# Kernel tuning notes

Hardware: AMD Instinct MI355X
Metric: run time of the kernel (lower is better)

The kernel has to match this reference:

```python
import jax, jax.numpy as jnp
import numpy as np

EPS = 1e-12  # F.normalize eps


def setup_inputs() -> dict:
    key = jax.random.key(0)
    k1, k2 = jax.random.split(key)
    bs, d = 8192, 128
    data = jax.random.normal(k1, (bs, d), dtype=jnp.float32)
    label = jax.random.randint(k2, (bs, 1), 0, 2, dtype=jnp.int64)
    scale = jnp.asarray(np.log(1.0 / 0.07), dtype=jnp.float32)  # learned temperature param
    return {"data": data, "scale": scale, "label": label}


def reference(data, scale, label):
    bs = data.shape[0]
    # L2-normalize rows (F.normalize semantics with eps clamp)
    norm = jnp.maximum(jnp.linalg.norm(data, axis=-1, keepdims=True), EPS)
    x = data / norm
    logits = (x @ x.T) * jnp.exp(scale)  # [bs, bs]
    # Vectorized equivalent of the python double loop: binary same-class matrix
    sim = (label == label.T).astype(logits.dtype)  # [bs, bs]
    q = jax.nn.softmax(sim / jnp.sum(sim, axis=-1, keepdims=True), axis=-1)
    p = jax.nn.log_softmax(logits, axis=-1)
    log_q = jnp.log(q)  # q > 0 always (softmax output)
    # F.kl_div(p, q, 'batchmean') = sum(q * (log q - p)) / bs
    loss1 = jnp.sum(q * (log_q - p)) / bs
    # F.kl_div(q.log(), p.exp(), 'batchmean') = sum(exp(p) * (p - log q)) / bs
    loss2 = jnp.sum(jnp.exp(p) * (p - log_q)) / bs
    return (loss1 + loss2) * 0.5
```

## Files before the change

kernel.cpp:

```cpp
#include <hip/hip_runtime.h>
#include <stdint.h>

#define BS 8192
#define DD 128
#define L2E 1.4426950408889634f
#define LN2 0.6931471805599453f

typedef __attribute__((ext_vector_type(8))) short short8;
typedef __attribute__((ext_vector_type(4))) float float4v;

#if __has_builtin(__builtin_amdgcn_exp2f)
#define EXP2(x) __builtin_amdgcn_exp2f(x)
#else
#define EXP2(x) exp2f(x)
#endif

__device__ __forceinline__ float bf2f(short s) {
  union { unsigned u; float f; } c;
  c.u = ((unsigned)(unsigned short)s) << 16;
  return c.f;
}
__device__ __forceinline__ short f2bf(float f) {
  union { float f; unsigned u; } c; c.f = f;
  unsigned u = c.u + 0x7FFFu + ((c.u >> 16) & 1u);
  return (short)(u >> 16);
}


__global__ __launch_bounds__(256) void k_norm(const float* __restrict__ data,
                                              const int* __restrict__ label,
                                              char* __restrict__ xnbF,
                                              float* __restrict__ Zr,
                                              float* __restrict__ Ur,
                                              float* __restrict__ Vr,
                                              float* __restrict__ Wr,
                                              float* __restrict__ Xr,
                                              float* __restrict__ mf) {
  int tid = threadIdx.x, wave = tid >> 6, lane = tid & 63;
  int lh = lane & 31, rsel = lane >> 5;
  int rowbase = blockIdx.x * 16;
  if (tid < 16) {
    int row = rowbase + tid;
    Zr[row] = 0.f; Ur[row] = 0.f; Vr[row] = 0.f; Wr[row] = 0.f; Xr[row] = 0.f;
    mf[row] = (label[row] == 0) ? 1.f : 0.f;
  }
#pragma unroll
  for (int it = 0; it < 2; ++it) {
    int row = rowbase + it * 8 + wave * 2 + rsel;
    float4 v = *(const float4*)&data[row * DD + lh * 4];
    float ss = v.x * v.x + v.y * v.y + v.z * v.z + v.w * v.w;
#pragma unroll
    for (int off = 16; off; off >>= 1) ss += __shfl_xor(ss, off);
    float rn = 1.f / fmaxf(sqrtf(ss), 1e-12f);
    float x0 = v.x * rn, x1 = v.y * rn, x2 = v.z * rn, x3 = v.w * rn;

    unsigned pk0 = (unsigned)(unsigned short)f2bf(x0) |
                   ((unsigned)(unsigned short)f2bf(x1) << 16);
    unsigned pk1 = (unsigned)(unsigned short)f2bf(x2) |
                   ((unsigned)(unsigned short)f2bf(x3) << 16);
    int kc = lh >> 1;
    size_t chunk = (size_t)(row >> 4) * 256 + (size_t)(kc >> 2) * 64 +
                   (size_t)(kc & 3) * 16 + (row & 15);
    *(uint2*)(xnbF + chunk * 16 + (lh & 1) * 8) = make_uint2(pk0, pk1);
  }
}

__global__ __launch_bounds__(512, 4) void k_main(const short* __restrict__ xnbF,
                                                 const int* __restrict__ label,
                                                 const float* __restrict__ mf,
                                                 const float* __restrict__ scale,
                                                 float* __restrict__ Zr,
                                                 float* __restrict__ Ur,
                                                 float* __restrict__ Vr,
                                                 float* __restrict__ Wr,
                                                 float* __restrict__ Xr,
                                                 int* __restrict__ ticket,
                                                 float* __restrict__ out) {
  __shared__ short tile[2][64 * DD];
  __shared__ int credu[8];
  __shared__ float fredu[8];
  __shared__ int lastf;
  int tid = threadIdx.x, wave = tid >> 6, lane = tid & 63;
  int quad = lane >> 4, col = lane & 15;
  int rbI = blockIdx.x >> 4;
  int sl = blockIdx.x & 15;
  float se2 = __expf(scale[0]) * L2E;

  const short8* F = (const short8*)xnbF;
  int gA = rbI * 16 + wave * 2;
  short8 af[2][4];
#pragma unroll
  for (int s = 0; s < 2; ++s)
#pragma unroll
    for (int t = 0; t < 4; ++t) {
      short8 a = F[(size_t)(gA + s) * 256 + t * 64 + lane];
#pragma unroll
      for (int i = 0; i < 8; ++i) a[i] = f2bf(bf2f(a[i]) * se2);
      af[s][t] = a;
    }

  float4v Z0 = {0.f,0.f,0.f,0.f}, Z1 = Z0, U0 = Z0, U1 = Z0, V0 = Z0, V1 = Z0;
  float4v W0 = Z0, W1 = Z0, X0 = Z0, X1 = Z0;
  int cb4 = sl * 32;

#define STAGE(buf, jt)                                                         \
  {                                                                            \
    const char* s_ = (const char*)xnbF +                                       \
                     ((size_t)(cb4 + (jt) * 4) * 256 + tid) * 16;              \
    char* d_ = (char*)tile[buf] + tid * 16;                                    \
    __builtin_amdgcn_global_load_lds(                                          \
        (const __attribute__((address_space(1))) void*)(uintptr_t)s_,          \
        (__attribute__((address_space(3))) void*)(uintptr_t)d_, 16, 0, 0);     \
    __builtin_amdgcn_global_load_lds(                                          \
        (const __attribute__((address_space(1))) void*)(uintptr_t)(s_ + 8192), \
        (__attribute__((address_space(3))) void*)(uintptr_t)(d_ + 8192),       \
        16, 0, 0);                                                             \
  }

  STAGE(0, 0);
  __syncthreads();

#pragma unroll 1
  for (int jt = 0; jt < 8; ++jt) {
    if (jt < 7) STAGE((jt + 1) & 1, jt + 1);
    const short8* T8 = (const short8*)tile[jt & 1];
    int jcb = sl * 512 + jt * 64;

#define HALFTILE(jo)                                                           \
    {                                                                          \
      short8 b00 = T8[(jo) * 256 + lane];                                      \
      short8 b01 = T8[(jo) * 256 + 64 + lane];                                 \
      short8 b02 = T8[(jo) * 256 + 128 + lane];                                \
      short8 b03 = T8[(jo) * 256 + 192 + lane];                                \
      short8 b10 = T8[(jo + 1) * 256 + lane];                                  \
      short8 b11 = T8[(jo + 1) * 256 + 64 + lane];                             \
      short8 b12 = T8[(jo + 1) * 256 + 128 + lane];                            \
      short8 b13 = T8[(jo + 1) * 256 + 192 + lane];                            \
      float m0 = mf[jcb + (jo) * 16 + col];                                    \
      float m1 = mf[jcb + (jo + 1) * 16 + col];                                \
      float4v c00 = {0.f, 0.f, 0.f, 0.f}, c01 = c00, c10 = c00, c11 = c00;     \
      c00 = __builtin_amdgcn_mfma_f32_16x16x32_bf16(af[0][0], b00, c00, 0,0,0);\
      c01 = __builtin_amdgcn_mfma_f32_16x16x32_bf16(af[1][0], b00, c01, 0,0,0);\
      c10 = __builtin_amdgcn_mfma_f32_16x16x32_bf16(af[0][0], b10, c10, 0,0,0);\
      c11 = __builtin_amdgcn_mfma_f32_16x16x32_bf16(af[1][0], b10, c11, 0,0,0);\
      c00 = __builtin_amdgcn_mfma_f32_16x16x32_bf16(af[0][1], b01, c00, 0,0,0);\
      c01 = __builtin_amdgcn_mfma_f32_16x16x32_bf16(af[1][1], b01, c01, 0,0,0);\
      c10 = __builtin_amdgcn_mfma_f32_16x16x32_bf16(af[0][1], b11, c10, 0,0,0);\
      c11 = __builtin_amdgcn_mfma_f32_16x16x32_bf16(af[1][1], b11, c11, 0,0,0);\
      c00 = __builtin_amdgcn_mfma_f32_16x16x32_bf16(af[0][2], b02, c00, 0,0,0);\
      c01 = __builtin_amdgcn_mfma_f32_16x16x32_bf16(af[1][2], b02, c01, 0,0,0);\
      c10 = __builtin_amdgcn_mfma_f32_16x16x32_bf16(af[0][2], b12, c10, 0,0,0);\
      c11 = __builtin_amdgcn_mfma_f32_16x16x32_bf16(af[1][2], b12, c11, 0,0,0);\
      c00 = __builtin_amdgcn_mfma_f32_16x16x32_bf16(af[0][3], b03, c00, 0,0,0);\
      c01 = __builtin_amdgcn_mfma_f32_16x16x32_bf16(af[1][3], b03, c01, 0,0,0);\
      c10 = __builtin_amdgcn_mfma_f32_16x16x32_bf16(af[0][3], b13, c10, 0,0,0);\
      c11 = __builtin_amdgcn_mfma_f32_16x16x32_bf16(af[1][3], b13, c11, 0,0,0);\
      _Pragma("unroll")                                                        \
      for (int r = 0; r < 4; ++r) {  \
        float l, e;                                                            \
        l = c00[r]; e = EXP2(l);        \
        Z0[r] += e; U0[r] = fmaf(e, l, U0[r]); V0[r] = fmaf(m0, e, V0[r]);     \
        W0[r] += l; X0[r] = fmaf(m0, l, X0[r]);                                \
        l = c01[r]; e = EXP2(l);                                               \
        Z1[r] += e; U1[r] = fmaf(e, l, U1[r]); V1[r] = fmaf(m0, e, V1[r]);     \
        W1[r] += l; X1[r] = fmaf(m0, l, X1[r]);                                \
        l = c10[r]; e = EXP2(l);                                               \
        Z0[r] += e; U0[r] = fmaf(e, l, U0[r]); V0[r] = fmaf(m1, e, V0[r]);     \
        W0[r] += l; X0[r] = fmaf(m1, l, X0[r]);                                \
        l = c11[r]; e = EXP2(l);                                               \
        Z1[r] += e; U1[r] = fmaf(e, l, U1[r]); V1[r] = fmaf(m1, e, V1[r]);     \
        W1[r] += l; X1[r] = fmaf(m1, l, X1[r]);                                \
      }                                                                        \
    }
    HALFTILE(0)
    HALFTILE(2)
#undef HALFTILE
    __syncthreads();
  }
#undef STAGE

#define EMIT(s, Zc, Uc, Vc, Wc, Xc)                                            \
  {                                                                            \
    _Pragma("unroll")                                                          \
    for (int r = 0; r < 4; ++r) {                                              \
      float z = Zc[r], u = Uc[r], v0 = Vc[r], w = Wc[r], x0 = Xc[r];           \
      _Pragma("unroll")                                                        \
      for (int off = 1; off < 16; off <<= 1) {                                 \
        z += __shfl_xor(z, off);                                               \
        u += __shfl_xor(u, off);                                               \
        v0 += __shfl_xor(v0, off);                                             \
        w += __shfl_xor(w, off);                                               \
        x0 += __shfl_xor(x0, off);                                             \
      }                                                                        \
      if (col == 0) {                                                          \
        int row = rbI * 256 + wave * 32 + s * 16 + quad * 4 + r;               \
        int lab = label[row];                                                  \
        float v = (lab == 0) ? v0 : (z - v0);                                  \
        float x = (lab == 0) ? x0 : (w - x0);                                  \
        atomicAdd(&Zr[row], z);                                                \
        atomicAdd(&Ur[row], u * LN2);                 \
        atomicAdd(&Vr[row], v);                                                \
        atomicAdd(&Wr[row], w * LN2);        \
        atomicAdd(&Xr[row], x * LN2);                         \
      }                                                                        \
    }                                                                          \
  }
  EMIT(0, Z0, U0, V0, W0, X0)
  EMIT(1, Z1, U1, V1, W1, X1)
#undef EMIT

  __syncthreads();
  if (tid == 0) {
    int t = __hip_atomic_fetch_add(ticket, 1, __ATOMIC_ACQ_REL,
                                   __HIP_MEMORY_SCOPE_AGENT);
    lastf = (t == 511);
  }
  __syncthreads();
  if (!lastf) return;

  int labs[16];
  int c1i = 0;
#pragma unroll
  for (int k = 0; k < 16; ++k) {
    labs[k] = label[k * 512 + tid];
    c1i += labs[k];
  }
#pragma unroll
  for (int off = 32; off; off >>= 1) c1i += __shfl_xor(c1i, off);
  if (lane == 0) credu[wave] = c1i;
  __syncthreads();
  int c1t = 0;
#pragma unroll
  for (int w = 0; w < 8; ++w) c1t += credu[w];
  float c1 = (float)c1t, c0 = (float)(BS - c1t);
  float a0 = __expf(1.f / c0), a1 = __expf(1.f / c1);
  float rZq0 = 1.f / (c0 * a0 + ((float)BS - c0));
  float rZq1 = 1.f / (c1 * a1 + ((float)BS - c1));
  float rc0 = 1.f / c0, rc1 = 1.f / c1;

  float local = 0.f;
#pragma unroll
  for (int k = 0; k < 16; ++k) {
    int row = k * 512 + tid;
    float Z = __hip_atomic_load(&Zr[row], __ATOMIC_RELAXED, __HIP_MEMORY_SCOPE_AGENT);
    float U = __hip_atomic_load(&Ur[row], __ATOMIC_RELAXED, __HIP_MEMORY_SCOPE_AGENT);
    float V = __hip_atomic_load(&Vr[row], __ATOMIC_RELAXED, __HIP_MEMORY_SCOPE_AGENT);
    float S = __hip_atomic_load(&Wr[row], __ATOMIC_RELAXED, __HIP_MEMORY_SCOPE_AGENT);
    float T = __hip_atomic_load(&Xr[row], __ATOMIC_RELAXED, __HIP_MEMORY_SCOPE_AGENT);
    int lab = labs[k];
    float a = lab ? a1 : a0;
    float rZq = lab ? rZq1 : rZq0;
    float rc = lab ? rc1 : rc0;
    local += rZq * (a - S - (a - 1.f) * T) + (U - V * rc) / Z;
  }
#pragma unroll
  for (int off = 32; off; off >>= 1) local += __shfl_xor(local, off);
  if (lane == 0) fredu[wave] = local;
  __syncthreads();
  if (tid == 0) {
    float s = 0.f;
#pragma unroll
    for (int w = 0; w < 8; ++w) s += fredu[w];
    out[0] = s * (0.5f / (float)BS);
  }
}

extern "C" void kernel_launch(void* const* d_in, const int* in_sizes, int n_in,
                              void* d_out, int out_size, void* d_ws, size_t ws_size,
                              hipStream_t stream) {
  const float* data = (const float*)d_in[0];
  const float* scale = (const float*)d_in[1];
  const int* label = (const int*)d_in[2];
  char* ws = (char*)d_ws;
  char* xnbF = ws;
  float* Zr = (float*)(ws + 2097152);
  float* Ur = (float*)(ws + 2129920);
  float* Vr = (float*)(ws + 2162688);
  float* Wr = (float*)(ws + 2195456);
  float* Xr = (float*)(ws + 2228224);
  float* mf = (float*)(ws + 2260992);
  int* ticket = (int*)(ws + 2293760);

  hipMemsetAsync(ws + 2293760, 0, 4, stream);

  k_norm<<<512, 256, 0, stream>>>(data, label, xnbF, Zr, Ur, Vr, Wr, Xr, mf);
  k_main<<<512, 512, 0, stream>>>((const short*)xnbF, label, mf, scale, Zr, Ur,
                                  Vr, Wr, Xr, ticket, (float*)d_out);
}
```

Baseline: 117.1 us.

## Replace per-element logit sums with class-sum vector dot products

The per-row sums of logits (W) and of same-class logits (X) are no longer accumulated inside the inner exp loop. They are rebuilt algebraically from per-class sums of the normalized rows, collected in k_norm through 16-way sharded atomics, and combined in the final block as dot products. This cuts two FMAs/adds per logit, two accumulator vectors, and two atomic outputs per row, which lowers register pressure in the hot loop. The cost is extra atomics in k_norm and a loss of precision, because the sums now use fp32 normalized vectors rather than the bf16 scaled GEMM results.

```diff
diff --git a/kernel.cpp b/kernel.cpp
--- a/kernel.cpp
+++ b/kernel.cpp
@@ -30,20 +30,25 @@
 __global__ __launch_bounds__(256) void k_norm(const float* __restrict__ data,
                                               const int* __restrict__ label,
                                               char* __restrict__ xnbF,
+                                              float* __restrict__ gh16,
                                               float* __restrict__ Zr,
                                               float* __restrict__ Ur,
                                               float* __restrict__ Vr,
-                                              float* __restrict__ Wr,
-                                              float* __restrict__ Xr,
                                               float* __restrict__ mf) {
+  __shared__ float shg[256];
   int tid = threadIdx.x, wave = tid >> 6, lane = tid & 63;
   int lh = lane & 31, rsel = lane >> 5;
+  shg[tid] = 0.f;
   int rowbase = blockIdx.x * 16;
   if (tid < 16) {
     int row = rowbase + tid;
-    Zr[row] = 0.f; Ur[row] = 0.f; Vr[row] = 0.f; Wr[row] = 0.f; Xr[row] = 0.f;
+    Zr[row] = 0.f; Ur[row] = 0.f; Vr[row] = 0.f;
     mf[row] = (label[row] == 0) ? 1.f : 0.f;
   }
+  __syncthreads();
+
+  float a00 = 0.f, a01 = 0.f, a02 = 0.f, a03 = 0.f;
+  float a10 = 0.f, a11 = 0.f, a12 = 0.f, a13 = 0.f;
 #pragma unroll
   for (int it = 0; it < 2; ++it) {
     int row = rowbase + it * 8 + wave * 2 + rsel;
@@ -62,23 +67,37 @@
     size_t chunk = (size_t)(row >> 4) * 256 + (size_t)(kc >> 2) * 64 +
                    (size_t)(kc & 3) * 16 + (row & 15);
     *(uint2*)(xnbF + chunk * 16 + (lh & 1) * 8) = make_uint2(pk0, pk1);
-  }
+
+    int lab = label[row];
+    if (lab == 0) {
+      a00 += x0; a01 += x1; a02 += x2; a03 += x3;
+    } else {
+      a10 += x0; a11 += x1; a12 += x2; a13 += x3;
+    }
+  }
+  int base = lh * 4;
+  atomicAdd(&shg[base + 0], a00); atomicAdd(&shg[base + 1], a01);
+  atomicAdd(&shg[base + 2], a02); atomicAdd(&shg[base + 3], a03);
+  atomicAdd(&shg[128 + base + 0], a10); atomicAdd(&shg[128 + base + 1], a11);
+  atomicAdd(&shg[128 + base + 2], a12); atomicAdd(&shg[128 + base + 3], a13);
+  __syncthreads();
+  atomicAdd(&gh16[(blockIdx.x & 15) * 256 + tid], shg[tid]);
 }
 
 __global__ __launch_bounds__(512, 4) void k_main(const short* __restrict__ xnbF,
                                                  const int* __restrict__ label,
                                                  const float* __restrict__ mf,
                                                  const float* __restrict__ scale,
+                                                 const float* __restrict__ gh16,
                                                  float* __restrict__ Zr,
                                                  float* __restrict__ Ur,
                                                  float* __restrict__ Vr,
-                                                 float* __restrict__ Wr,
-                                                 float* __restrict__ Xr,
                                                  int* __restrict__ ticket,
                                                  float* __restrict__ out) {
   __shared__ short tile[2][64 * DD];
   __shared__ int credu[8];
   __shared__ float fredu[8];
+  __shared__ float dred[24];
   __shared__ int lastf;
   int tid = threadIdx.x, wave = tid >> 6, lane = tid & 63;
   int quad = lane >> 4, col = lane & 15;
@@ -100,7 +119,6 @@
     }
 
   float4v Z0 = {0.f,0.f,0.f,0.f}, Z1 = Z0, U0 = Z0, U1 = Z0, V0 = Z0, V1 = Z0;
-  float4v W0 = Z0, W1 = Z0, X0 = Z0, X1 = Z0;
   int cb4 = sl * 32;
 
 #define STAGE(buf, jt)                                                         \
@@ -160,16 +178,12 @@
         float l, e;                                                            \
         l = c00[r]; e = EXP2(l);        \
         Z0[r] += e; U0[r] = fmaf(e, l, U0[r]); V0[r] = fmaf(m0, e, V0[r]);     \
-        W0[r] += l; X0[r] = fmaf(m0, l, X0[r]);                                \
         l = c01[r]; e = EXP2(l);                                               \
         Z1[r] += e; U1[r] = fmaf(e, l, U1[r]); V1[r] = fmaf(m0, e, V1[r]);     \
-        W1[r] += l; X1[r] = fmaf(m0, l, X1[r]);                                \
         l = c10[r]; e = EXP2(l);                                               \
         Z0[r] += e; U0[r] = fmaf(e, l, U0[r]); V0[r] = fmaf(m1, e, V0[r]);     \
-        W0[r] += l; X0[r] = fmaf(m1, l, X0[r]);                                \
         l = c11[r]; e = EXP2(l);                                               \
         Z1[r] += e; U1[r] = fmaf(e, l, U1[r]); V1[r] = fmaf(m1, e, V1[r]);     \
-        W1[r] += l; X1[r] = fmaf(m1, l, X1[r]);                                \
       }                                                                        \
     }
     HALFTILE(0)
@@ -179,34 +193,29 @@
   }
 #undef STAGE
 
-#define EMIT(s, Zc, Uc, Vc, Wc, Xc)                                            \
+#define EMIT(s, Zc, Uc, Vc)                                                    \
   {                                                                            \
     _Pragma("unroll")                                                          \
     for (int r = 0; r < 4; ++r) {                                              \
-      float z = Zc[r], u = Uc[r], v0 = Vc[r], w = Wc[r], x0 = Xc[r];           \
+      float z = Zc[r], u = Uc[r], v0 = Vc[r];                                  \
       _Pragma("unroll")                                                        \
       for (int off = 1; off < 16; off <<= 1) {                                 \
         z += __shfl_xor(z, off);                                               \
         u += __shfl_xor(u, off);                                               \
         v0 += __shfl_xor(v0, off);                                             \
-        w += __shfl_xor(w, off);                                               \
-        x0 += __shfl_xor(x0, off);                                             \
       }                                                                        \
       if (col == 0) {                                                          \
         int row = rbI * 256 + wave * 32 + s * 16 + quad * 4 + r;               \
         int lab = label[row];                                                  \
         float v = (lab == 0) ? v0 : (z - v0);                                  \
-        float x = (lab == 0) ? x0 : (w - x0);                                  \
         atomicAdd(&Zr[row], z);                                                \
         atomicAdd(&Ur[row], u * LN2);                 \
         atomicAdd(&Vr[row], v);                                                \
-        atomicAdd(&Wr[row], w * LN2);        \
-        atomicAdd(&Xr[row], x * LN2);                         \
       }                                                                        \
     }                                                                          \
   }
-  EMIT(0, Z0, U0, V0, W0, X0)
-  EMIT(1, Z1, U1, V1, W1, X1)
+  EMIT(0, Z0, U0, V0)
+  EMIT(1, Z1, U1, V1)
 #undef EMIT
 
   __syncthreads();
@@ -218,13 +227,16 @@
   __syncthreads();
   if (!lastf) return;
 
-  int labs[16];
+  float* hs = (float*)tile;
+  if (tid < 256) {
+    float h = 0.f;
+#pragma unroll
+    for (int i = 0; i < 16; ++i) h += gh16[i * 256 + tid];
+    hs[tid] = h;
+  }
   int c1i = 0;
 #pragma unroll
-  for (int k = 0; k < 16; ++k) {
-    labs[k] = label[k * 512 + tid];
-    c1i += labs[k];
-  }
+  for (int k = 0; k < 16; ++k) c1i += label[k * 512 + tid];
 #pragma unroll
   for (int off = 32; off; off >>= 1) c1i += __shfl_xor(c1i, off);
   if (lane == 0) credu[wave] = c1i;
@@ -233,35 +245,49 @@
 #pragma unroll
   for (int w = 0; w < 8; ++w) c1t += credu[w];
   float c1 = (float)c1t, c0 = (float)(BS - c1t);
-  float a0 = __expf(1.f / c0), a1 = __expf(1.f / c1);
-  float rZq0 = 1.f / (c0 * a0 + ((float)BS - c0));
-  float rZq1 = 1.f / (c1 * a1 + ((float)BS - c1));
+
+  float p00 = 0.f, p01 = 0.f, p11 = 0.f;
+  if (tid < 128) {
+    float h0d = hs[tid], h1d = hs[128 + tid];
+    p00 = h0d * h0d; p01 = h0d * h1d; p11 = h1d * h1d;
+  }
+#pragma unroll
+  for (int off = 32; off; off >>= 1) {
+    p00 += __shfl_xor(p00, off);
+    p01 += __shfl_xor(p01, off);
+    p11 += __shfl_xor(p11, off);
+  }
+  if (lane == 0) { dred[wave] = p00; dred[8 + wave] = p01; dred[16 + wave] = p11; }
+
   float rc0 = 1.f / c0, rc1 = 1.f / c1;
-
   float local = 0.f;
 #pragma unroll
   for (int k = 0; k < 16; ++k) {
     int row = k * 512 + tid;
+    int lab = label[row];
     float Z = __hip_atomic_load(&Zr[row], __ATOMIC_RELAXED, __HIP_MEMORY_SCOPE_AGENT);
     float U = __hip_atomic_load(&Ur[row], __ATOMIC_RELAXED, __HIP_MEMORY_SCOPE_AGENT);
     float V = __hip_atomic_load(&Vr[row], __ATOMIC_RELAXED, __HIP_MEMORY_SCOPE_AGENT);
-    float S = __hip_atomic_load(&Wr[row], __ATOMIC_RELAXED, __HIP_MEMORY_SCOPE_AGENT);
-    float T = __hip_atomic_load(&Xr[row], __ATOMIC_RELAXED, __HIP_MEMORY_SCOPE_AGENT);
-    int lab = labs[k];
-    float a = lab ? a1 : a0;
-    float rZq = lab ? rZq1 : rZq0;
-    float rc = lab ? rc1 : rc0;
-    local += rZq * (a - S - (a - 1.f) * T) + (U - V * rc) / Z;
+    local += (U - V * (lab ? rc1 : rc0)) / Z;
   }
 #pragma unroll
   for (int off = 32; off; off >>= 1) local += __shfl_xor(local, off);
   if (lane == 0) fredu[wave] = local;
   __syncthreads();
   if (tid == 0) {
-    float s = 0.f;
-#pragma unroll
-    for (int w = 0; w < 8; ++w) s += fredu[w];
-    out[0] = s * (0.5f / (float)BS);
+    float se = __expf(scale[0]);
+    float a0 = __expf(1.f / c0), a1 = __expf(1.f / c1);
+    float rZq0 = 1.f / (c0 * a0 + ((float)BS - c0));
+    float rZq1 = 1.f / (c1 * a1 + ((float)BS - c1));
+    float d00 = dred[0] + dred[1], d01 = dred[8] + dred[9],
+          d11 = dred[16] + dred[17];
+    float rows = 0.f;
+#pragma unroll
+    for (int w = 0; w < 8; ++w) rows += fredu[w];
+    float stsum = se * (rZq0 * ((d00 + d01) + (a0 - 1.f) * d00) +
+                        rZq1 * ((d01 + d11) + (a1 - 1.f) * d11));
+    float total = c0 * a0 * rZq0 + c1 * a1 * rZq1 - stsum + rows;
+    out[0] = total * (0.5f / (float)BS);
   }
 }
 
@@ -276,14 +302,13 @@
   float* Zr = (float*)(ws + 2097152);
   float* Ur = (float*)(ws + 2129920);
   float* Vr = (float*)(ws + 2162688);
-  float* Wr = (float*)(ws + 2195456);
-  float* Xr = (float*)(ws + 2228224);
-  float* mf = (float*)(ws + 2260992);
-  int* ticket = (int*)(ws + 2293760);
-
-  hipMemsetAsync(ws + 2293760, 0, 4, stream);
-
-  k_norm<<<512, 256, 0, stream>>>(data, label, xnbF, Zr, Ur, Vr, Wr, Xr, mf);
-  k_main<<<512, 512, 0, stream>>>((const short*)xnbF, label, mf, scale, Zr, Ur,
-                                  Vr, Wr, Xr, ticket, (float*)d_out);
-}
+  float* gh16 = (float*)(ws + 2195456);
+  int* ticket = (int*)(ws + 2211840);
+  float* mf = (float*)(ws + 2211872);
+
+  hipMemsetAsync(ws + 2195456, 0, 16388, stream);
+
+  k_norm<<<512, 256, 0, stream>>>(data, label, xnbF, gh16, Zr, Ur, Vr, mf);
+  k_main<<<512, 512, 0, stream>>>((const short*)xnbF, label, mf, scale, gh16,
+                                  Zr, Ur, Vr, ticket, (float*)d_out);
+}
```

Result: faster. 102.9 us (median of 3 runs) (-12.1%).
